# Kernel optimization log

Measured on AMD Instinct MI355X. Metric: run time of the kernel, lower is better.

The kernel has to match this reference:

```python
import jax, jax.numpy as jnp
import numpy as np

HIDDEN = 640
NQ = 10      # query heads
NKV = 2      # kv heads
HD = HIDDEN // NQ   # 64
GROUPS = NQ // NKV  # 5
THETA = 500000.0
EPS = 1e-6


def rmsnorm(x, g):
    rms = jnp.sqrt(jnp.mean(x * x, axis=-1, keepdims=True) + EPS)
    return x / rms * g


def bitlinear(x, w, g):
    """RMSNorm + ternary weight / int8 activation fake-quant + GEMM + rescale."""
    x = rmsnorm(x, g)
    alpha = jnp.maximum(jnp.mean(jnp.abs(w)), 1e-10)
    w_q = jnp.clip(jnp.round(w / alpha), -1.0, 1.0)
    w_q = w + jax.lax.stop_gradient(w_q - w)            # STE
    gamma = jnp.maximum(jnp.max(jnp.abs(x), axis=-1, keepdims=True), 1e-10)
    x_q = jnp.clip(jnp.round(x * 127.0 / gamma), -128.0, 127.0)
    x_q = x + jax.lax.stop_gradient(x_q - x)            # STE
    return (x_q @ w_q.T) * (alpha * gamma / 127.0)


def rope_tables(L):
    # half-dim cos/sin tables [L, HD//2]; equivalent to the torch code's
    # repeat_interleave followed by [..., ::2] slicing.
    freqs = 1.0 / THETA ** (jnp.arange(0, HD, 2, dtype=jnp.float32) / HD)
    ang = jnp.arange(L, dtype=jnp.float32)[:, None] * freqs[None, :]
    return jnp.cos(ang), jnp.sin(ang)


def apply_rope(x, cos, sin):
    # x: [B,H,L,D]; cos/sin: [L,D/2] broadcast over B,H
    x1 = x[..., ::2]
    x2 = x[..., 1::2]
    o1 = x1 * cos - x2 * sin
    o2 = x2 * cos + x1 * sin
    return jnp.stack([o1, o2], axis=-1).reshape(x.shape)


def setup_inputs() -> dict:
    key = jax.random.key(0)
    ks = jax.random.split(key, 6)
    B, L = 32, 512
    x = jax.random.normal(ks[0], (B, L, HIDDEN), dtype=jnp.float32)
    s_h = 1.0 / np.sqrt(HIDDEN)
    q_w = jax.random.normal(ks[1], (NQ * HD, HIDDEN), dtype=jnp.float32) * s_h
    k_w = jax.random.normal(ks[2], (NKV * HD, HIDDEN), dtype=jnp.float32) * s_h
    v_w = jax.random.normal(ks[3], (NKV * HD, HIDDEN), dtype=jnp.float32) * s_h
    o_w = jax.random.normal(ks[4], (HIDDEN, NQ * HD), dtype=jnp.float32) * (1.0 / np.sqrt(NQ * HD))
    ones = jnp.ones((HIDDEN,), dtype=jnp.float32)
    return {
        "x": x,
        "norm_w": ones,
        "q_w": q_w, "q_g": ones,
        "k_w": k_w, "k_g": ones,
        "v_w": v_w, "v_g": ones,
        "o_w": o_w, "o_g": jnp.ones((NQ * HD,), dtype=jnp.float32),
    }


def reference(x, norm_w, q_w, q_g, k_w, k_g, v_w, v_g, o_w, o_g):
    B, L, _ = x.shape
    residual = x
    h = rmsnorm(x, norm_w)
    q = bitlinear(h, q_w, q_g).reshape(B, L, NQ, HD).transpose(0, 2, 1, 3)
    k = bitlinear(h, k_w, k_g).reshape(B, L, NKV, HD).transpose(0, 2, 1, 3)
    v = bitlinear(h, v_w, v_g).reshape(B, L, NKV, HD).transpose(0, 2, 1, 3)
    cos, sin = rope_tables(L)
    q = apply_rope(q, cos, sin)
    k = apply_rope(k, cos, sin)
    k = jnp.repeat(k, GROUPS, axis=1)   # [B,NQ,L,HD]
    v = jnp.repeat(v, GROUPS, axis=1)
    scale = 1.0 / np.sqrt(HD).astype(np.float32)
    attn = jnp.einsum("bhqd,bhkd->bhqk", q, k) * scale
    attn = jax.nn.softmax(attn, axis=-1)
    out = jnp.einsum("bhqk,bhkd->bhqd", attn, v)
    out = out.transpose(0, 2, 1, 3).reshape(B, L, NQ * HD)
    return bitlinear(out, o_w, o_g) + residual
```

## Files before the change

### kernel.cpp

```cpp
#include <hip/hip_runtime.h>
#include <math.h>
#include <stdint.h>

#define HIDDEN 640
#define NTOK   16384
#define LSEQ   512
#define BATCH  32
#define NQH    10
#define NKVH   2
#define HDIM   64
#define GROUPS 5

typedef int      int4v  __attribute__((ext_vector_type(4)));
typedef int      int16v __attribute__((ext_vector_type(16)));
typedef _Float16 f16x8  __attribute__((ext_vector_type(8)));
typedef _Float16 f16x2  __attribute__((ext_vector_type(2)));
typedef float    f32x4  __attribute__((ext_vector_type(4)));

__device__ __forceinline__ float wred_sum(float v){
  #pragma unroll
  for (int m=1;m<64;m<<=1) v += __shfl_xor(v,m);
  return v;
}
__device__ __forceinline__ float wred_max(float v){
  #pragma unroll
  for (int m=1;m<64;m<<=1) v = fmaxf(v,__shfl_xor(v,m));
  return v;
}

__device__ __forceinline__ int frag_flat(int m, int k){
  return (((m>>5)*20 + (k>>5))<<10) + (((((k>>4)&1)<<5) | (m&31))<<4) + (k&15);
}

__global__ __launch_bounds__(256) void absum4_kernel(
    const float* __restrict__ w0, const float* __restrict__ w1,
    const float* __restrict__ w2, const float* __restrict__ w3,
    float* __restrict__ sums){
  const float* w; int n;
  switch(blockIdx.y){
    case 0:  w=w0; n=640*640; break;
    case 1:  w=w1; n=128*640; break;
    case 2:  w=w2; n=128*640; break;
    default: w=w3; n=640*640; break;
  }
  __shared__ float red[256];
  int tid = threadIdx.x;
  float s = 0.f;
  for (int i = blockIdx.x*256 + tid; i < n; i += gridDim.x*256) s += fabsf(w[i]);
  red[tid] = s; __syncthreads();
  for (int off=128; off>0; off>>=1){ if (tid<off) red[tid]+=red[tid+off]; __syncthreads(); }
  if (tid==0) atomicAdd(&sums[blockIdx.y], red[0]);
}

__global__ __launch_bounds__(256) void wquant4_kernel(
    const float* __restrict__ w0, const float* __restrict__ w1,
    const float* __restrict__ w2, const float* __restrict__ w3,
    int8_t* __restrict__ o0, int8_t* __restrict__ o1,
    int8_t* __restrict__ o2, int8_t* __restrict__ o3,
    const float* __restrict__ sums){
  const float* w; int8_t* o; int n;
  switch(blockIdx.y){
    case 0:  w=w0; o=o0; n=640*640; break;
    case 1:  w=w1; o=o1; n=128*640; break;
    case 2:  w=w2; o=o2; n=128*640; break;
    default: w=w3; o=o3; n=640*640; break;
  }
  float alpha = fmaxf(sums[blockIdx.y]/(float)n, 1e-10f);
  float inva  = 1.0f/alpha;
  int i = blockIdx.x*256 + threadIdx.x;
  if (i < n){
    float t = rintf(w[i]*inva);
    t = fminf(1.f, fmaxf(-1.f, t));
    int nr = i/640;
    int kc = i - nr*640;
    o[frag_flat(nr, kc)] = (int8_t)t;
  }
}

__global__ __launch_bounds__(256) void token_prep_kernel(
    const float* __restrict__ x, const float* __restrict__ nw,
    const float* __restrict__ qg, const float* __restrict__ kg, const float* __restrict__ vg,
    int8_t* __restrict__ xqq, int8_t* __restrict__ xqk, int8_t* __restrict__ xqv,
    float* __restrict__ gq, float* __restrict__ gk, float* __restrict__ gv){
  int lane = threadIdx.x & 63;
  int m = blockIdx.x*4 + (threadIdx.x>>6);
  const float* xr = x + (size_t)m*HIDDEN;
  int abase = ((m>>5)*20480) + ((m&31)<<4)
            + ((lane>>5)<<10) + (((lane>>4)&1)<<9) + (lane&15);
  float xv[10], h[10];
  float ss = 0.f;
  #pragma unroll
  for (int j=0;j<10;j++){ float t = xr[lane + 64*j]; xv[j]=t; ss += t*t; }
  float inv1 = 1.0f/sqrtf(wred_sum(ss)*(1.0f/HIDDEN) + 1e-6f);
  float ss2 = 0.f;
  #pragma unroll
  for (int j=0;j<10;j++){ float t = xv[j]*inv1*nw[lane+64*j]; h[j]=t; ss2 += t*t; }
  float inv2 = 1.0f/sqrtf(wred_sum(ss2)*(1.0f/HIDDEN) + 1e-6f);

  const float* gs[3] = {qg, kg, vg};
  int8_t* outs[3] = {xqq, xqk, xqv};
  float* gams[3] = {gq, gk, gv};
  #pragma unroll
  for (int s=0;s<3;s++){
    const float* g = gs[s];
    float t[10], amax = 0.f;
    #pragma unroll
    for (int j=0;j<10;j++){ float v = h[j]*inv2*g[lane+64*j]; t[j]=v; amax = fmaxf(amax, fabsf(v)); }
    float gamma = fmaxf(wred_max(amax), 1e-10f);
    float sc = 127.0f/gamma;
    int8_t* dst = outs[s] + abase;
    #pragma unroll
    for (int j=0;j<10;j++){
      float v = rintf(t[j]*sc);
      v = fminf(127.f, fmaxf(-128.f, v));
      dst[j*2048] = (int8_t)v;
    }
    if (lane==0) gams[s][m] = gamma;
  }
}

__global__ __launch_bounds__(256) void o_prep_kernel(const _Float16* __restrict__ ao,
    const float* __restrict__ og, int8_t* __restrict__ xqo, float* __restrict__ go){
  int lane = threadIdx.x & 63;
  int m = blockIdx.x*4 + (threadIdx.x>>6);
  const _Float16* xr = ao + (size_t)m*HIDDEN;
  int abase = ((m>>5)*20480) + ((m&31)<<4)
            + ((lane>>5)<<10) + (((lane>>4)&1)<<9) + (lane&15);
  float xv[10];
  float ss = 0.f;
  #pragma unroll
  for (int j=0;j<10;j++){ float t = (float)xr[lane + 64*j]; xv[j]=t; ss += t*t; }
  float inv = 1.0f/sqrtf(wred_sum(ss)*(1.0f/HIDDEN) + 1e-6f);
  float t[10], amax = 0.f;
  #pragma unroll
  for (int j=0;j<10;j++){ float v = xv[j]*inv*og[lane+64*j]; t[j]=v; amax = fmaxf(amax, fabsf(v)); }
  float gamma = fmaxf(wred_max(amax), 1e-10f);
  float sc = 127.0f/gamma;
  int8_t* dst = xqo + abase;
  #pragma unroll
  for (int j=0;j<10;j++){
    float v = rintf(t[j]*sc);
    v = fminf(127.f, fmaxf(-128.f, v));
    dst[j*2048] = (int8_t)v;
  }
  if (lane==0) go[m] = gamma;
}

__device__ __forceinline__ void gemm_core(
    const int8_t* __restrict__ xq, const int8_t* __restrict__ wqf,
    int m0, int n0, int lane, int16v& acc0, int16v& acc1){
  const int8_t* a0 = xq  + (size_t)(m0>>5)*20480 + (lane<<4);
  const int8_t* b0 = wqf + (size_t)(n0>>5)*20480 + (lane<<4);
  const int8_t* b1 = b0 + 20480;
  #pragma unroll
  for (int kb=0; kb<20; kb++){
    int4v a  = *(const int4v*)(a0 + (kb<<10));
    int4v v0 = *(const int4v*)(b0 + (kb<<10));
    int4v v1 = *(const int4v*)(b1 + (kb<<10));
    acc0 = __builtin_amdgcn_mfma_i32_32x32x32_i8(a, v0, acc0, 0, 0, 0);
    acc1 = __builtin_amdgcn_mfma_i32_32x32x32_i8(a, v1, acc1, 0, 0, 0);
  }
}

__global__ __launch_bounds__(256) void qkv_gemm_kernel(
    const int8_t* __restrict__ xq_q, const float* __restrict__ g_q, const int8_t* __restrict__ wq_q,
    const int8_t* __restrict__ xq_k, const float* __restrict__ g_k, const int8_t* __restrict__ wq_k,
    const int8_t* __restrict__ xq_v, const float* __restrict__ g_v, const int8_t* __restrict__ wq_v,
    const float* __restrict__ sums,
    _Float16* __restrict__ qbuf, _Float16* __restrict__ kbuf, _Float16* __restrict__ vbuf){
  __shared__ _Float16 Tr[4][64][40];
  int bx = blockIdx.x;
  const int8_t *xq, *wq; const float* gam; _Float16* outh;
  int n0, aidx, nheads, mode; float inv_nw, vscale;
  if (bx < 10){ xq=xq_q; wq=wq_q; gam=g_q; outh=qbuf; n0=bx*64;      aidx=0; inv_nw=1.0f/409600.f; nheads=NQH;  mode=1; vscale=0.18033688011110918f; }
  else if (bx < 12){ xq=xq_k; wq=wq_k; gam=g_k; outh=kbuf; n0=(bx-10)*64; aidx=1; inv_nw=1.0f/81920.f; nheads=NKVH; mode=1; vscale=1.0f; }
  else { xq=xq_v; wq=wq_v; gam=g_v; outh=vbuf; n0=(bx-12)*64; aidx=2; inv_nw=1.0f/81920.f; nheads=NKVH; mode=2; vscale=1.0f; }

  int lane = threadIdx.x & 63;
  int w    = threadIdx.x >> 6;
  int m0   = blockIdx.y*128 + w*32;
  int half = lane >> 5, lan5 = lane & 31;

  int16v acc0 = {0}, acc1 = {0};
  gemm_core(xq, wq, m0, n0, lane, acc0, acc1);

  float alpha = fmaxf(sums[aidx]*inv_nw, 1e-10f);
  float fr0 = 0.f, fr1 = 0.f;
  if (mode == 1){
    int d0 = (lan5) & ~1;
    int d1 = (32 + lan5) & ~1;
    fr0 = __expf(-(float)d0*(1.0f/64.0f)*13.122363377404328f);
    fr1 = __expf(-(float)d1*(1.0f/64.0f)*13.122363377404328f);
  }

  #pragma unroll
  for (int reg=0; reg<16; reg++){
    int ml = (reg&3) + 8*(reg>>2) + 4*half;
    int m = m0 + ml;
    float sc = alpha*gam[m]*(1.0f/127.0f);
    float v0 = (float)acc0[reg]*sc;
    float v1 = (float)acc1[reg]*sc;
    if (mode == 1){
      int b = m >> 9, l = m & 511;
      int head = n0 >> 6;
      float p0 = __shfl_xor(v0, 1);
      float p1 = __shfl_xor(v1, 1);
      float sn0, cs0, sn1, cs1;
      __sincosf((float)l*fr0, &sn0, &cs0);
      __sincosf((float)l*fr1, &sn1, &cs1);
      if (lane & 1){ v0 = v0*cs0 + p0*sn0;  v1 = v1*cs1 + p1*sn1; }
      else         { v0 = v0*cs0 - p0*sn0;  v1 = v1*cs1 - p1*sn1; }
      _Float16* dst = outh + ((((size_t)b*nheads + head)*LSEQ + l)<<6);
      dst[lan5]      = (_Float16)(v0*vscale);
      dst[32 + lan5] = (_Float16)(v1*vscale);
    } else {
      Tr[w][lan5][ml]      = (_Float16)v0;
      Tr[w][32 + lan5][ml] = (_Float16)v1;
    }
  }
  if (mode == 2){
    int b = m0 >> 9, l0 = m0 & 511;
    int head = n0 >> 6;
    f16x8 r0 = *(const f16x8*)&Tr[w][lane][0];
    f16x8 r1 = *(const f16x8*)&Tr[w][lane][8];
    f16x8 r2 = *(const f16x8*)&Tr[w][lane][16];
    f16x8 r3 = *(const f16x8*)&Tr[w][lane][24];
    _Float16* dst = outh + (((size_t)b*nheads + head)*HDIM + lane)*LSEQ + l0;
    ((f16x8*)dst)[0] = r0;
    ((f16x8*)dst)[1] = r1;
    ((f16x8*)dst)[2] = r2;
    ((f16x8*)dst)[3] = r3;
  }
}

__global__ __launch_bounds__(256) void out_gemm_kernel(
    const int8_t* __restrict__ xq, const float* __restrict__ gam,
    const int8_t* __restrict__ wq, const float* __restrict__ sums,
    const float* __restrict__ resid, float* __restrict__ outf){
  int lane = threadIdx.x & 63;
  int w    = threadIdx.x >> 6;
  int m0   = blockIdx.y*128 + w*32;
  int n0   = blockIdx.x*64;
  int half = lane >> 5, lan5 = lane & 31;

  int16v acc0 = {0}, acc1 = {0};
  gemm_core(xq, wq, m0, n0, lane, acc0, acc1);

  float alpha = fmaxf(sums[3]*(1.0f/409600.f), 1e-10f);
  #pragma unroll
  for (int reg=0; reg<16; reg++){
    int m = m0 + (reg&3) + 8*(reg>>2) + 4*half;
    float sc = alpha*gam[m]*(1.0f/127.0f);
    size_t ofs = (size_t)m*HIDDEN;
    outf[ofs + n0 + lan5]      = (float)acc0[reg]*sc + resid[ofs + n0 + lan5];
    outf[ofs + n0 + 32 + lan5] = (float)acc1[reg]*sc + resid[ofs + n0 + 32 + lan5];
  }
}

__device__ __forceinline__ int kv_addr(int row, int chunk){
  return (row<<6) + (((chunk ^ (row&7)))<<3);
}

__device__ __forceinline__ void softmax_half(
    const f32x4* S, float& m, f32x4& lacc, f32x4* O, int quad, bool first,
    f16x8& pf0, f16x8& pf1){
  float t0 = fmaxf(fmaxf(S[0][0],S[0][1]), fmaxf(S[0][2],S[0][3]));
  float t1 = fmaxf(fmaxf(S[1][0],S[1][1]), fmaxf(S[1][2],S[1][3]));
  float t2 = fmaxf(fmaxf(S[2][0],S[2][1]), fmaxf(S[2][2],S[2][3]));
  float t3 = fmaxf(fmaxf(S[3][0],S[3][1]), fmaxf(S[3][2],S[3][3]));
  float tmax = fmaxf(fmaxf(t0,t1), fmaxf(t2,t3));
  float p[16];
  if (first || __any(tmax > 8.0f)){
    float rmax = fmaxf(tmax, __shfl_xor(tmax, 16));
    rmax = fmaxf(rmax, __shfl_xor(rmax, 32));
    float delta = first ? rmax : fmaxf(rmax, 0.0f);
    m += delta;
    float af = exp2f(-delta);
    #pragma unroll
    for (int r=0;r<4;r++){
      float afr = __shfl(af, (quad<<2)+r);
      lacc[r] *= afr;
      O[0][r]*=afr; O[1][r]*=afr; O[2][r]*=afr; O[3][r]*=afr;
    }
    #pragma unroll
    for (int nt=0;nt<4;nt++){
      #pragma unroll
      for (int j=0;j<4;j++) p[(nt<<2)+j] = exp2f(S[nt][j] - delta);
    }
  } else {
    #pragma unroll
    for (int nt=0;nt<4;nt++){
      #pragma unroll
      for (int j=0;j<4;j++) p[(nt<<2)+j] = exp2f(S[nt][j]);
    }
  }
  uint32_t W[4][2];
  #pragma unroll
  for (int nt=0;nt<4;nt++){
    W[nt][0] = __builtin_bit_cast(uint32_t,
                 __builtin_amdgcn_cvt_pkrtz(p[(nt<<2)+0], p[(nt<<2)+1]));
    W[nt][1] = __builtin_bit_cast(uint32_t,
                 __builtin_amdgcn_cvt_pkrtz(p[(nt<<2)+2], p[(nt<<2)+3]));
  }
  #pragma unroll
  for (int pp=0;pp<2;pp++){
    asm volatile("v_permlane32_swap_b32 %0, %1" : "+v"(W[0][pp]), "+v"(W[1][pp]));
    asm volatile("v_permlane32_swap_b32 %0, %1" : "+v"(W[2][pp]), "+v"(W[3][pp]));
    asm volatile("v_permlane16_swap_b32 %0, %1" : "+v"(W[0][pp]), "+v"(W[1][pp]));
    asm volatile("v_permlane16_swap_b32 %0, %1" : "+v"(W[2][pp]), "+v"(W[3][pp]));
  }
  union { uint32_t u[4]; f16x8 v; } a, b;
  a.u[0]=W[0][0]; a.u[1]=W[0][1]; a.u[2]=W[1][0]; a.u[3]=W[1][1];
  b.u[0]=W[2][0]; b.u[1]=W[2][1]; b.u[2]=W[3][0]; b.u[3]=W[3][1];
  pf0 = a.v; pf1 = b.v;
}

__global__ __launch_bounds__(256,3) void attn_mfma_kernel(
    const _Float16* __restrict__ q, const _Float16* __restrict__ k,
    const _Float16* __restrict__ vt, _Float16* __restrict__ o){
  __shared__ _Float16 Ks[2][64*64];
  __shared__ _Float16 Vs[2][64*64];
  int tid  = threadIdx.x;
  int wv   = tid >> 6, lane = tid & 63;
  int quad = lane >> 4, c = lane & 15;
  int h = blockIdx.y, b = blockIdx.z;
  int hk = h / GROUPS;
  int qrow0 = blockIdx.x*128 + wv*32;
  (void)wv;

  const _Float16* qb = q + ((size_t)((b*NQH+h)*LSEQ) + qrow0 + c)*HDIM + quad*8;
  f16x8 qa0 = *(const f16x8*)qb;
  f16x8 qa1 = *(const f16x8*)(qb + 32);
  f16x8 qb0 = *(const f16x8*)(qb + 16*HDIM);
  f16x8 qb1 = *(const f16x8*)(qb + 16*HDIM + 32);

  const _Float16* kbase = k  + (size_t)((b*NKVH+hk)*LSEQ)*HDIM;
  const _Float16* vbase = vt + (size_t)((b*NKVH+hk)*HDIM)*LSEQ;

  int srow = tid >> 3, schunk = tid & 7;
  const _Float16* kg0 = kbase + (size_t)srow*HDIM      + schunk*8;
  const _Float16* kg1 = kbase + (size_t)(srow+32)*HDIM + schunk*8;
  const _Float16* vg0 = vbase + (size_t)srow*LSEQ      + schunk*8;
  const _Float16* vg1 = vbase + (size_t)(srow+32)*LSEQ + schunk*8;
  int ka0 = kv_addr(srow,    schunk);
  int ka1 = kv_addr(srow+32, schunk);

  {
    f16x8 t0 = *(const f16x8*)kg0;
    f16x8 t1 = *(const f16x8*)kg1;
    f16x8 t2 = *(const f16x8*)vg0;
    f16x8 t3 = *(const f16x8*)vg1;
    *(f16x8*)&Ks[0][ka0] = t0;
    *(f16x8*)&Ks[0][ka1] = t1;
    *(f16x8*)&Vs[0][ka0] = t2;
    *(f16x8*)&Vs[0][ka1] = t3;
  }

  f32x4 O0[4] = {{0,0,0,0},{0,0,0,0},{0,0,0,0},{0,0,0,0}};
  f32x4 O1[4] = {{0,0,0,0},{0,0,0,0},{0,0,0,0},{0,0,0,0}};
  f32x4 lacc0 = {0,0,0,0}, lacc1 = {0,0,0,0};
  float m0s = 0.f, m1s = 0.f;
  const f16x8 ones = {(_Float16)1.f,(_Float16)1.f,(_Float16)1.f,(_Float16)1.f,
                      (_Float16)1.f,(_Float16)1.f,(_Float16)1.f,(_Float16)1.f};
  f16x8 pk0, pk1, pv0, pv1;

  for (int kt=0; kt<8; kt++){
    __syncthreads();
    int cur = kt & 1, nxt = cur ^ 1;
    if (kt < 7){
      pk0 = *(const f16x8*)(kg0 + (size_t)(kt+1)*64*HDIM);
      pk1 = *(const f16x8*)(kg1 + (size_t)(kt+1)*64*HDIM);
      pv0 = *(const f16x8*)(vg0 + (kt+1)*64);
      pv1 = *(const f16x8*)(vg1 + (kt+1)*64);
    }
    f32x4 S0[4], S1[4];
    __builtin_amdgcn_s_setprio(1);
    #pragma unroll
    for (int nt=0; nt<4; nt++){
      int row = (nt<<4) + c;
      f16x8 kf0 = *(const f16x8*)&Ks[cur][kv_addr(row, quad)];
      f16x8 kf1 = *(const f16x8*)&Ks[cur][kv_addr(row, quad+4)];
      f32x4 s = {-m0s,-m0s,-m0s,-m0s};
      s = __builtin_amdgcn_mfma_f32_16x16x32_f16(kf0, qa0, s, 0,0,0);
      s = __builtin_amdgcn_mfma_f32_16x16x32_f16(kf1, qa1, s, 0,0,0);
      S0[nt] = s;
      f32x4 s2 = {-m1s,-m1s,-m1s,-m1s};
      s2 = __builtin_amdgcn_mfma_f32_16x16x32_f16(kf0, qb0, s2, 0,0,0);
      s2 = __builtin_amdgcn_mfma_f32_16x16x32_f16(kf1, qb1, s2, 0,0,0);
      S1[nt] = s2;
    }
    __builtin_amdgcn_s_setprio(0);
    f16x8 pf00, pf01, pf10, pf11;
    softmax_half(S0, m0s, lacc0, O0, quad, kt==0, pf00, pf01);
    softmax_half(S1, m1s, lacc1, O1, quad, kt==0, pf10, pf11);
    __builtin_amdgcn_s_setprio(1);
    lacc0 = __builtin_amdgcn_mfma_f32_16x16x32_f16(pf00, ones, lacc0, 0,0,0);
    lacc0 = __builtin_amdgcn_mfma_f32_16x16x32_f16(pf01, ones, lacc0, 0,0,0);
    lacc1 = __builtin_amdgcn_mfma_f32_16x16x32_f16(pf10, ones, lacc1, 0,0,0);
    lacc1 = __builtin_amdgcn_mfma_f32_16x16x32_f16(pf11, ones, lacc1, 0,0,0);
    #pragma unroll
    for (int nt=0;nt<4;nt++){
      int row = (nt<<4) + c;
      f16x8 vf0 = *(const f16x8*)&Vs[cur][kv_addr(row, quad)];
      f16x8 vf1 = *(const f16x8*)&Vs[cur][kv_addr(row, quad+4)];
      O0[nt] = __builtin_amdgcn_mfma_f32_16x16x32_f16(pf00, vf0, O0[nt], 0,0,0);
      O0[nt] = __builtin_amdgcn_mfma_f32_16x16x32_f16(pf01, vf1, O0[nt], 0,0,0);
      O1[nt] = __builtin_amdgcn_mfma_f32_16x16x32_f16(pf10, vf0, O1[nt], 0,0,0);
      O1[nt] = __builtin_amdgcn_mfma_f32_16x16x32_f16(pf11, vf1, O1[nt], 0,0,0);
    }
    __builtin_amdgcn_s_setprio(0);
    if (kt < 7){
      *(f16x8*)&Ks[nxt][ka0] = pk0;
      *(f16x8*)&Ks[nxt][ka1] = pk1;
      *(f16x8*)&Vs[nxt][ka0] = pv0;
      *(f16x8*)&Vs[nxt][ka1] = pv1;
    }
  }
  #pragma unroll
  for (int r=0;r<4;r++){
    float invl0 = 1.0f/lacc0[r];
    float invl1 = 1.0f/lacc1[r];
    int m0 = (b<<9) + qrow0 + (quad<<2) + r;
    _Float16* d0 = o + (size_t)m0*HIDDEN + (h<<6);
    _Float16* d1 = o + (size_t)(m0+16)*HIDDEN + (h<<6);
    #pragma unroll
    for (int nt=0;nt<4;nt++){
      d0[(nt<<4)+c] = (_Float16)(O0[nt][r]*invl0);
      d1[(nt<<4)+c] = (_Float16)(O1[nt][r]*invl1);
    }
  }
}

extern "C" void kernel_launch(void* const* d_in, const int* in_sizes, int n_in,
                              void* d_out, int out_size, void* d_ws, size_t ws_size,
                              hipStream_t stream){
  (void)in_sizes; (void)n_in; (void)out_size; (void)ws_size;
  const float* x  = (const float*)d_in[0];
  const float* nw = (const float*)d_in[1];
  const float* qw = (const float*)d_in[2];
  const float* qg = (const float*)d_in[3];
  const float* kw = (const float*)d_in[4];
  const float* kg = (const float*)d_in[5];
  const float* vw = (const float*)d_in[6];
  const float* vg = (const float*)d_in[7];
  const float* ow = (const float*)d_in[8];
  const float* og = (const float*)d_in[9];
  float* out = (float*)d_out;

  char* base = (char*)d_ws;
  size_t off = 0;
  auto alloc = [&](size_t nbytes)->void*{
    off = (off + 255) & ~(size_t)255;
    void* p = base + off;
    off += nbytes;
    return p;
  };
  float*  sums = (float*) alloc(4*sizeof(float));
  int8_t* wq_q = (int8_t*)alloc(640*640);
  int8_t* wq_k = (int8_t*)alloc(128*640);
  int8_t* wq_v = (int8_t*)alloc(128*640);
  int8_t* wq_o = (int8_t*)alloc(640*640);
  int8_t* xq_q = (int8_t*)alloc((size_t)NTOK*HIDDEN);
  int8_t* xq_k = (int8_t*)alloc((size_t)NTOK*HIDDEN);
  int8_t* xq_v = (int8_t*)alloc((size_t)NTOK*HIDDEN);
  int8_t* xq_o = (int8_t*)alloc((size_t)NTOK*HIDDEN);
  float*  g_q  = (float*) alloc((size_t)NTOK*4);
  float*  g_k  = (float*) alloc((size_t)NTOK*4);
  float*  g_v  = (float*) alloc((size_t)NTOK*4);
  float*  g_o  = (float*) alloc((size_t)NTOK*4);
  _Float16* qbuf = (_Float16*)alloc((size_t)BATCH*NQH *LSEQ*HDIM*2);
  _Float16* kbuf = (_Float16*)alloc((size_t)BATCH*NKVH*LSEQ*HDIM*2);
  _Float16* vbuf = (_Float16*)alloc((size_t)BATCH*NKVH*LSEQ*HDIM*2);
  _Float16* abuf = (_Float16*)alloc((size_t)NTOK*HIDDEN*2);

  (void)hipMemsetAsync(sums, 0, 4*sizeof(float), stream);
  absum4_kernel<<<dim3(64,4),256,0,stream>>>(qw, kw, vw, ow, sums);
  wquant4_kernel<<<dim3(1600,4),256,0,stream>>>(qw, kw, vw, ow, wq_q, wq_k, wq_v, wq_o, sums);

  token_prep_kernel<<<NTOK/4,256,0,stream>>>(x, nw, qg, kg, vg, xq_q, xq_k, xq_v, g_q, g_k, g_v);

  qkv_gemm_kernel<<<dim3(14,128),256,0,stream>>>(xq_q, g_q, wq_q,
                                                 xq_k, g_k, wq_k,
                                                 xq_v, g_v, wq_v,
                                                 sums, qbuf, kbuf, vbuf);

  attn_mfma_kernel<<<dim3(4,NQH,BATCH),256,0,stream>>>(qbuf, kbuf, vbuf, abuf);

  o_prep_kernel<<<NTOK/4,256,0,stream>>>(abuf, og, xq_o, g_o);
  out_gemm_kernel<<<dim3(10,128),256,0,stream>>>(xq_o, g_o, wq_o, sums, x, out);
}
```

Baseline: 240.3 us.

## Vectorize token prep loads and stores; remap attention grid for KV-head L2 locality

The token and o-projection prep kernels now load pairs of floats or halves and write two int8 values per 16-bit store, using a new fragment address mapping for adjacent k columns. This is meant to cut the number of narrow global memory transactions. The attention launch changes to a 1D grid whose block index is decoded so that the 8 blocks spaced 8 apart (likely landing on different XCDs) cover different batch/KV-head groups, while each group's 20 blocks (5 query heads × 4 row tiles) stay on one XCD and reuse that KV head's K/V from its L2. The risk is that the new address maps are wrong, which would corrupt layout or coverage.

```diff
diff --git a/kernel.cpp b/kernel.cpp
--- a/kernel.cpp
+++ b/kernel.cpp
@@ -16,6 +16,7 @@
 typedef _Float16 f16x8  __attribute__((ext_vector_type(8)));
 typedef _Float16 f16x2  __attribute__((ext_vector_type(2)));
 typedef float    f32x4  __attribute__((ext_vector_type(4)));
+typedef float    f32x2  __attribute__((ext_vector_type(2)));
 
 __device__ __forceinline__ float wred_sum(float v){
   #pragma unroll
@@ -30,6 +31,11 @@
 
 __device__ __forceinline__ int frag_flat(int m, int k){
   return (((m>>5)*20 + (k>>5))<<10) + (((((k>>4)&1)<<5) | (m&31))<<4) + (k&15);
+}
+
+__device__ __forceinline__ int frag_pair_base(int m, int lane){
+  return ((m>>5)*20480) + ((m&31)<<4)
+       + ((lane>>4)<<10) + (((lane>>3)&1)<<9) + ((lane&7)<<1);
 }
 
 __global__ __launch_bounds__(256) void absum4_kernel(
@@ -84,17 +90,24 @@
     float* __restrict__ gq, float* __restrict__ gk, float* __restrict__ gv){
   int lane = threadIdx.x & 63;
   int m = blockIdx.x*4 + (threadIdx.x>>6);
-  const float* xr = x + (size_t)m*HIDDEN;
-  int abase = ((m>>5)*20480) + ((m&31)<<4)
-            + ((lane>>5)<<10) + (((lane>>4)&1)<<9) + (lane&15);
-  float xv[10], h[10];
+  const f32x2* xr  = (const f32x2*)(x + (size_t)m*HIDDEN);
+  const f32x2* nw2 = (const f32x2*)nw;
+  int pbase = frag_pair_base(m, lane);
+  f32x2 xv[5], h[5];
   float ss = 0.f;
   #pragma unroll
-  for (int j=0;j<10;j++){ float t = xr[lane + 64*j]; xv[j]=t; ss += t*t; }
+  for (int jj=0;jj<5;jj++){
+    f32x2 t = xr[lane + 64*jj];
+    xv[jj]=t; ss += t.x*t.x + t.y*t.y;
+  }
   float inv1 = 1.0f/sqrtf(wred_sum(ss)*(1.0f/HIDDEN) + 1e-6f);
   float ss2 = 0.f;
   #pragma unroll
-  for (int j=0;j<10;j++){ float t = xv[j]*inv1*nw[lane+64*j]; h[j]=t; ss2 += t*t; }
+  for (int jj=0;jj<5;jj++){
+    f32x2 w = nw2[lane + 64*jj];
+    f32x2 t; t.x = xv[jj].x*inv1*w.x; t.y = xv[jj].y*inv1*w.y;
+    h[jj]=t; ss2 += t.x*t.x + t.y*t.y;
+  }
   float inv2 = 1.0f/sqrtf(wred_sum(ss2)*(1.0f/HIDDEN) + 1e-6f);
 
   const float* gs[3] = {qg, kg, vg};
@@ -102,18 +115,25 @@
   float* gams[3] = {gq, gk, gv};
   #pragma unroll
   for (int s=0;s<3;s++){
-    const float* g = gs[s];
-    float t[10], amax = 0.f;
-    #pragma unroll
-    for (int j=0;j<10;j++){ float v = h[j]*inv2*g[lane+64*j]; t[j]=v; amax = fmaxf(amax, fabsf(v)); }
+    const f32x2* g2 = (const f32x2*)gs[s];
+    f32x2 t[5]; float amax = 0.f;
+    #pragma unroll
+    for (int jj=0;jj<5;jj++){
+      f32x2 g = g2[lane + 64*jj];
+      f32x2 v; v.x = h[jj].x*inv2*g.x; v.y = h[jj].y*inv2*g.y;
+      t[jj]=v;
+      amax = fmaxf(amax, fmaxf(fabsf(v.x), fabsf(v.y)));
+    }
     float gamma = fmaxf(wred_max(amax), 1e-10f);
     float sc = 127.0f/gamma;
-    int8_t* dst = outs[s] + abase;
-    #pragma unroll
-    for (int j=0;j<10;j++){
-      float v = rintf(t[j]*sc);
-      v = fminf(127.f, fmaxf(-128.f, v));
-      dst[j*2048] = (int8_t)v;
+    int8_t* dst = outs[s] + pbase;
+    #pragma unroll
+    for (int jj=0;jj<5;jj++){
+      float q0 = fminf(127.f, fmaxf(-128.f, rintf(t[jj].x*sc)));
+      float q1 = fminf(127.f, fmaxf(-128.f, rintf(t[jj].y*sc)));
+      uint16_t pk = (uint16_t)(uint8_t)(int8_t)q0
+                  | ((uint16_t)(uint8_t)(int8_t)q1 << 8);
+      *(uint16_t*)(dst + jj*4096) = pk;
     }
     if (lane==0) gams[s][m] = gamma;
   }
@@ -123,25 +143,36 @@
     const float* __restrict__ og, int8_t* __restrict__ xqo, float* __restrict__ go){
   int lane = threadIdx.x & 63;
   int m = blockIdx.x*4 + (threadIdx.x>>6);
-  const _Float16* xr = ao + (size_t)m*HIDDEN;
-  int abase = ((m>>5)*20480) + ((m&31)<<4)
-            + ((lane>>5)<<10) + (((lane>>4)&1)<<9) + (lane&15);
-  float xv[10];
+  const uint32_t* xr2 = (const uint32_t*)(ao + (size_t)m*HIDDEN);
+  const f32x2* og2 = (const f32x2*)og;
+  int pbase = frag_pair_base(m, lane);
+  f32x2 xv[5];
   float ss = 0.f;
   #pragma unroll
-  for (int j=0;j<10;j++){ float t = (float)xr[lane + 64*j]; xv[j]=t; ss += t*t; }
+  for (int jj=0;jj<5;jj++){
+    f16x2 hp = __builtin_bit_cast(f16x2, xr2[lane + 64*jj]);
+    f32x2 t; t.x = (float)hp.x; t.y = (float)hp.y;
+    xv[jj]=t; ss += t.x*t.x + t.y*t.y;
+  }
   float inv = 1.0f/sqrtf(wred_sum(ss)*(1.0f/HIDDEN) + 1e-6f);
-  float t[10], amax = 0.f;
-  #pragma unroll
-  for (int j=0;j<10;j++){ float v = xv[j]*inv*og[lane+64*j]; t[j]=v; amax = fmaxf(amax, fabsf(v)); }
+  f32x2 t[5]; float amax = 0.f;
+  #pragma unroll
+  for (int jj=0;jj<5;jj++){
+    f32x2 g = og2[lane + 64*jj];
+    f32x2 v; v.x = xv[jj].x*inv*g.x; v.y = xv[jj].y*inv*g.y;
+    t[jj]=v;
+    amax = fmaxf(amax, fmaxf(fabsf(v.x), fabsf(v.y)));
+  }
   float gamma = fmaxf(wred_max(amax), 1e-10f);
   float sc = 127.0f/gamma;
-  int8_t* dst = xqo + abase;
-  #pragma unroll
-  for (int j=0;j<10;j++){
-    float v = rintf(t[j]*sc);
-    v = fminf(127.f, fmaxf(-128.f, v));
-    dst[j*2048] = (int8_t)v;
+  int8_t* dst = xqo + pbase;
+  #pragma unroll
+  for (int jj=0;jj<5;jj++){
+    float q0 = fminf(127.f, fmaxf(-128.f, rintf(t[jj].x*sc)));
+    float q1 = fminf(127.f, fmaxf(-128.f, rintf(t[jj].y*sc)));
+    uint16_t pk = (uint16_t)(uint8_t)(int8_t)q0
+                | ((uint16_t)(uint8_t)(int8_t)q1 << 8);
+    *(uint16_t*)(dst + jj*4096) = pk;
   }
   if (lane==0) go[m] = gamma;
 }
@@ -323,10 +354,16 @@
   int tid  = threadIdx.x;
   int wv   = tid >> 6, lane = tid & 63;
   int quad = lane >> 4, c = lane & 15;
-  int h = blockIdx.y, b = blockIdx.z;
-  int hk = h / GROUPS;
-  int qrow0 = blockIdx.x*128 + wv*32;
-  (void)wv;
+  int wgid = blockIdx.x;
+  int r8 = wgid & 7;
+  int j  = wgid >> 3;
+  int gslot = j / 20;
+  int s  = j - gslot*20;
+  int g  = gslot*8 + r8;
+  int b  = g >> 1;
+  int hk = g & 1;
+  int h  = hk*5 + (s >> 2);
+  int qrow0 = (s & 3)*128 + wv*32;
 
   const _Float16* qb = q + ((size_t)((b*NQH+h)*LSEQ) + qrow0 + c)*HDIM + quad*8;
   f16x8 qa0 = *(const f16x8*)qb;
@@ -380,10 +417,10 @@
       int row = (nt<<4) + c;
       f16x8 kf0 = *(const f16x8*)&Ks[cur][kv_addr(row, quad)];
       f16x8 kf1 = *(const f16x8*)&Ks[cur][kv_addr(row, quad+4)];
-      f32x4 s = {-m0s,-m0s,-m0s,-m0s};
-      s = __builtin_amdgcn_mfma_f32_16x16x32_f16(kf0, qa0, s, 0,0,0);
-      s = __builtin_amdgcn_mfma_f32_16x16x32_f16(kf1, qa1, s, 0,0,0);
-      S0[nt] = s;
+      f32x4 s0i = {-m0s,-m0s,-m0s,-m0s};
+      s0i = __builtin_amdgcn_mfma_f32_16x16x32_f16(kf0, qa0, s0i, 0,0,0);
+      s0i = __builtin_amdgcn_mfma_f32_16x16x32_f16(kf1, qa1, s0i, 0,0,0);
+      S0[nt] = s0i;
       f32x4 s2 = {-m1s,-m1s,-m1s,-m1s};
       s2 = __builtin_amdgcn_mfma_f32_16x16x32_f16(kf0, qb0, s2, 0,0,0);
       s2 = __builtin_amdgcn_mfma_f32_16x16x32_f16(kf1, qb1, s2, 0,0,0);
@@ -484,7 +521,7 @@
                                                  xq_v, g_v, wq_v,
                                                  sums, qbuf, kbuf, vbuf);
 
-  attn_mfma_kernel<<<dim3(4,NQH,BATCH),256,0,stream>>>(qbuf, kbuf, vbuf, abuf);
+  attn_mfma_kernel<<<dim3(1280),256,0,stream>>>(qbuf, kbuf, vbuf, abuf);
 
   o_prep_kernel<<<NTOK/4,256,0,stream>>>(abuf, og, xq_o, g_o);
   out_gemm_kernel<<<dim3(10,128),256,0,stream>>>(xq_o, g_o, wq_o, sums, x, out);
```

After: 243.3 us. About the same (+1.2%).
